# Optimization experiments

Hardware: AMD Instinct MI355X
Metric: run time of the kernel (lower is better)

The kernel has to match this reference:

```python
import jax, jax.numpy as jnp
import numpy as np

B, N = 2048, 4096

def setup_inputs() -> dict:
    key = jax.random.key(0)
    k1, k2, k3, k4, k5 = jax.random.split(key, 5)
    scale = 1.0 / np.sqrt(N)  # match nn.Linear init scale
    return {
        "t": jnp.zeros((1,), dtype=jnp.float32),
        "y": jax.random.uniform(k1, (B, N), dtype=jnp.float32),
        "W1": jax.random.normal(k2, (N, N), dtype=jnp.float32) * scale,
        "b1": jax.random.normal(k3, (N,), dtype=jnp.float32) * scale,
        "W2": jax.random.normal(k4, (N, N), dtype=jnp.float32) * scale,
        "b2": jax.random.normal(k5, (N,), dtype=jnp.float32) * scale,
    }

def reference(t, y, W1, b1, W2, b2):
    # out = fcc2(fcc1(y)) : two Linear layers (y @ W^T + b)
    h = y @ W1.T + b1            # [B, N]
    out = h @ W2.T + b2          # [B, N]
    # f = ones(N,1) @ y @ out^T  ==  dot(y, out) broadcast over N;
    # dydt = y * (out - dot(y, out))   (replicator equation)
    dot = jnp.sum(y * out, axis=-1, keepdims=True)  # [B, 1]
    return y * (out - dot)       # [B, N]
```

## Files before the change

### kernel.cpp

```cpp
#include <hip/hip_runtime.h>
#include <hip/hip_bf16.h>
#include <stdint.h>

typedef _Float16 f16;
typedef _Float16 f16x4 __attribute__((ext_vector_type(4)));
typedef _Float16 f16x8 __attribute__((ext_vector_type(8)));
typedef float f32x4 __attribute__((ext_vector_type(4)));

#define ASYNC_COPY16(gsrc, ldst)                                                   \
    __builtin_amdgcn_global_load_lds(                                              \
        (__attribute__((address_space(1))) void*)(gsrc),                           \
        (__attribute__((address_space(3))) void*)(ldst), 16, 0, 0)

__global__ __launch_bounds__(256) void cvt_f32_to_f16(const float* __restrict__ in,
                                                      f16* __restrict__ out, int n4) {
    int i = blockIdx.x * 256 + threadIdx.x;
    if (i >= n4) return;
    float4 v = ((const float4*)in)[i];
    f16x4 o;
    o.x = (f16)v.x; o.y = (f16)v.y; o.z = (f16)v.z; o.w = (f16)v.w;
    ((f16x4*)out)[i] = o;
}

__global__ __launch_bounds__(256) void cvt3_f32_to_f16(const float* __restrict__ y,
                                                       const float* __restrict__ W1,
                                                       const float* __restrict__ W2,
                                                       f16* __restrict__ yb,
                                                       f16* __restrict__ w1b,
                                                       f16* __restrict__ w2b,
                                                       int nY4, int nW4) {
    int i = blockIdx.x * 256 + threadIdx.x;
    const float* src;
    f16* dst;
    int off;
    if (i < nY4) {
        src = y; dst = yb; off = i;
    } else if (i < nY4 + nW4) {
        src = W1; dst = w1b; off = i - nY4;
    } else {
        src = W2; dst = w2b; off = i - nY4 - nW4;
        if (off >= nW4) return;
    }
    float4 v = ((const float4*)src)[off];
    f16x4 o;
    o.x = (f16)v.x; o.y = (f16)v.y; o.z = (f16)v.z; o.w = (f16)v.w;
    ((f16x4*)dst)[off] = o;
}

template <int STORE_F16>
__global__ __launch_bounds__(128) void gemm_bt(const f16* __restrict__ A,
                                               const f16* __restrict__ Bm,
                                               const float* __restrict__ bias,
                                               void* __restrict__ Cout,
                                               int M, int N, int K) {
    constexpr int BM = 128, BN = 64, BK = 32;
    __shared__ __align__(16) f16 sA[BM * BK];
    __shared__ __align__(16) f16 sB[BN * BK];

    const int tid  = threadIdx.x;
    const int lane = tid & 63;
    const int wave = tid >> 6;

    const int bm = blockIdx.y * BM;
    const int bn = blockIdx.x * BN;

    const int srow = tid >> 2;
    const int scol = (tid & 3) * 8;

    const f16* Aptr = A + (size_t)bm * K;
    const f16* Bptr = Bm + (size_t)bn * K;

    f32x4 acc[4][4] = {};

    const int quad = lane >> 4;
    const int l16  = lane & 15;

    for (int k0 = 0; k0 < K; k0 += BK) {
#pragma unroll
        for (int i = 0; i < 4; i++) {
            const int r = srow + 32 * i;
            ASYNC_COPY16(Aptr + (size_t)r * K + k0 + scol, &sA[r * BK + scol]);
        }
#pragma unroll
        for (int j = 0; j < 2; j++) {
            const int r = srow + 32 * j;
            ASYNC_COPY16(Bptr + (size_t)r * K + k0 + scol, &sB[r * BK + scol]);
        }
        __syncthreads();

        f16x8 af[4], bf[4];
#pragma unroll
        for (int mi = 0; mi < 4; mi++)
            af[mi] = *(const f16x8*)&sA[(wave * 64 + mi * 16 + l16) * BK + quad * 8];
#pragma unroll
        for (int ni = 0; ni < 4; ni++)
            bf[ni] = *(const f16x8*)&sB[(ni * 16 + l16) * BK + quad * 8];

#pragma unroll
        for (int mi = 0; mi < 4; mi++)
#pragma unroll
            for (int ni = 0; ni < 4; ni++)
                acc[mi][ni] = __builtin_amdgcn_mfma_f32_16x16x32_f16(af[mi], bf[ni],
                                                                     acc[mi][ni], 0, 0, 0);
        __syncthreads();
    }

#pragma unroll
    for (int ni = 0; ni < 4; ni++) {
        const int col = bn + ni * 16 + l16;
        const float bv = bias[col];
#pragma unroll
        for (int mi = 0; mi < 4; mi++) {
            const int row0 = bm + wave * 64 + mi * 16 + quad * 4;
#pragma unroll
            for (int r = 0; r < 4; r++) {
                float v = acc[mi][ni][r] + bv;
                if (STORE_F16)
                    ((f16*)Cout)[(size_t)(row0 + r) * N + col] = (f16)v;
                else
                    ((float*)Cout)[(size_t)(row0 + r) * N + col] = v;
            }
        }
    }
}

__global__ __launch_bounds__(256) void replicator(const float* __restrict__ y,
                                                  float* __restrict__ out, int N) {
    const int row = blockIdx.x;
    const float4* y4 = (const float4*)(y + (size_t)row * N);
    float4* o4 = (float4*)(out + (size_t)row * N);
    const int n4 = N / 4;

    float p = 0.f;
    for (int i = threadIdx.x; i < n4; i += 256) {
        float4 a = y4[i], b = o4[i];
        p += a.x * b.x + a.y * b.y + a.z * b.z + a.w * b.w;
    }
#pragma unroll
    for (int off = 32; off > 0; off >>= 1) p += __shfl_down(p, off, 64);

    __shared__ float sred[4];
    if ((threadIdx.x & 63) == 0) sred[threadIdx.x >> 6] = p;
    __syncthreads();
    const float dot = sred[0] + sred[1] + sred[2] + sred[3];

    for (int i = threadIdx.x; i < n4; i += 256) {
        float4 a = y4[i], b = o4[i];
        float4 r;
        r.x = a.x * (b.x - dot);
        r.y = a.y * (b.y - dot);
        r.z = a.z * (b.z - dot);
        r.w = a.w * (b.w - dot);
        o4[i] = r;
    }
}

extern "C" void kernel_launch(void* const* d_in, const int* in_sizes, int n_in,
                              void* d_out, int out_size, void* d_ws, size_t ws_size,
                              hipStream_t stream) {
    const float* y  = (const float*)d_in[1];
    const float* W1 = (const float*)d_in[2];
    const float* b1 = (const float*)d_in[3];
    const float* W2 = (const float*)d_in[4];
    const float* b2 = (const float*)d_in[5];

    const int N = in_sizes[3];
    const int B = in_sizes[1] / N;
    float* out = (float*)d_out;

    const size_t szY = (size_t)B * N;
    const size_t szW = (size_t)N * N;

    const int yn4 = (int)(szY / 4);
    const int wn4 = (int)(szW / 4);

    dim3 g1(N / 64, B / 128);

    const size_t need_big = (szY + 2 * szW + szY) * sizeof(f16);

    if (ws_size >= need_big) {
        f16* yb  = (f16*)d_ws;
        f16* w1b = yb + szY;
        f16* w2b = w1b + szW;
        f16* hb  = w2b + szW;

        const int tot4 = yn4 + 2 * wn4;
        cvt3_f32_to_f16<<<(tot4 + 255) / 256, 256, 0, stream>>>(y, W1, W2, yb, w1b, w2b,
                                                                yn4, wn4);
        gemm_bt<1><<<g1, 128, 0, stream>>>(yb, w1b, b1, hb, B, N, N);
        gemm_bt<0><<<g1, 128, 0, stream>>>(hb, w2b, b2, out, B, N, N);
    } else {
        f16* yb = (f16*)d_ws;
        f16* wb = yb + szY;
        f16* hb = wb + szW;

        cvt_f32_to_f16<<<yn4 / 256, 256, 0, stream>>>(y, yb, yn4);
        cvt_f32_to_f16<<<wn4 / 256, 256, 0, stream>>>(W1, wb, wn4);
        gemm_bt<1><<<g1, 128, 0, stream>>>(yb, wb, b1, hb, B, N, N);
        cvt_f32_to_f16<<<wn4 / 256, 256, 0, stream>>>(W2, wb, wn4);
        gemm_bt<0><<<g1, 128, 0, stream>>>(hb, wb, b2, out, B, N, N);
    }

    replicator<<<B, 256, 0, stream>>>(y, out, N);
}
```

Before: 433.3 us.

## Enlarge GEMM tiles, double-buffer LDS, and XOR-swizzle shared memory layout

The GEMM kernel moves from 128x64x32 tiles with 2 waves to 128x128x64 tiles with 4 waves in a 2x2 arrangement. LDS buffers are double-buffered so the async global-to-LDS copy of the next K-slice is issued before computing on the current one, removing one barrier per iteration. Shared memory segments are XOR-swizzled by row to avoid bank conflicts on the fragment reads. In exchange, LDS use and register pressure go up, and the grid has half as many blocks.

```diff
diff --git a/kernel.cpp b/kernel.cpp
--- a/kernel.cpp
+++ b/kernel.cpp
@@ -48,70 +48,106 @@
 }
 
 template <int STORE_F16>
-__global__ __launch_bounds__(128) void gemm_bt(const f16* __restrict__ A,
+__global__ __launch_bounds__(256) void gemm_bt(const f16* __restrict__ A,
                                                const f16* __restrict__ Bm,
                                                const float* __restrict__ bias,
                                                void* __restrict__ Cout,
                                                int M, int N, int K) {
-    constexpr int BM = 128, BN = 64, BK = 32;
-    __shared__ __align__(16) f16 sA[BM * BK];
-    __shared__ __align__(16) f16 sB[BN * BK];
-
-    const int tid  = threadIdx.x;
-    const int lane = tid & 63;
-    const int wave = tid >> 6;
+    constexpr int BM = 128, BN = 128, BK = 64;
+    __shared__ __align__(16) f16 sA[2][BM * BK];
+    __shared__ __align__(16) f16 sB[2][BN * BK];
+
+    const int tid   = threadIdx.x;
+    const int lane  = tid & 63;
+    const int wave  = tid >> 6;
+    const int waveM = wave >> 1;
+    const int waveN = wave & 1;
 
     const int bm = blockIdx.y * BM;
     const int bn = blockIdx.x * BN;
 
-    const int srow = tid >> 2;
-    const int scol = (tid & 3) * 8;
-
     const f16* Aptr = A + (size_t)bm * K;
     const f16* Bptr = Bm + (size_t)bn * K;
 
+    const int srow_lo = tid >> 3;
+    const int sseg    = tid & 7;
+
     f32x4 acc[4][4] = {};
 
     const int quad = lane >> 4;
     const int l16  = lane & 15;
 
-    for (int k0 = 0; k0 < K; k0 += BK) {
-#pragma unroll
-        for (int i = 0; i < 4; i++) {
-            const int r = srow + 32 * i;
-            ASYNC_COPY16(Aptr + (size_t)r * K + k0 + scol, &sA[r * BK + scol]);
-        }
-#pragma unroll
-        for (int j = 0; j < 2; j++) {
-            const int r = srow + 32 * j;
-            ASYNC_COPY16(Bptr + (size_t)r * K + k0 + scol, &sB[r * BK + scol]);
-        }
+    const int iters = K / BK;
+
+    {
+#pragma unroll
+        for (int j = 0; j < 4; j++) {
+            const int row = j * 32 + srow_lo;
+            const int seg = sseg ^ (row & 7);
+            ASYNC_COPY16(Aptr + (size_t)row * K + 0 + seg * 8, &sA[0][j * 2048 + tid * 8]);
+        }
+#pragma unroll
+        for (int j = 0; j < 4; j++) {
+            const int row = j * 32 + srow_lo;
+            const int seg = sseg ^ (row & 7);
+            ASYNC_COPY16(Bptr + (size_t)row * K + 0 + seg * 8, &sB[0][j * 2048 + tid * 8]);
+        }
+    }
+
+    int cur = 0;
+    for (int it = 0; it < iters; ++it) {
         __syncthreads();
 
-        f16x8 af[4], bf[4];
-#pragma unroll
-        for (int mi = 0; mi < 4; mi++)
-            af[mi] = *(const f16x8*)&sA[(wave * 64 + mi * 16 + l16) * BK + quad * 8];
-#pragma unroll
-        for (int ni = 0; ni < 4; ni++)
-            bf[ni] = *(const f16x8*)&sB[(ni * 16 + l16) * BK + quad * 8];
-
-#pragma unroll
-        for (int mi = 0; mi < 4; mi++)
-#pragma unroll
-            for (int ni = 0; ni < 4; ni++)
-                acc[mi][ni] = __builtin_amdgcn_mfma_f32_16x16x32_f16(af[mi], bf[ni],
-                                                                     acc[mi][ni], 0, 0, 0);
-        __syncthreads();
+        if (it + 1 < iters) {
+            const int k0 = (it + 1) * BK;
+#pragma unroll
+            for (int j = 0; j < 4; j++) {
+                const int row = j * 32 + srow_lo;
+                const int seg = sseg ^ (row & 7);
+                ASYNC_COPY16(Aptr + (size_t)row * K + k0 + seg * 8,
+                             &sA[cur ^ 1][j * 2048 + tid * 8]);
+            }
+#pragma unroll
+            for (int j = 0; j < 4; j++) {
+                const int row = j * 32 + srow_lo;
+                const int seg = sseg ^ (row & 7);
+                ASYNC_COPY16(Bptr + (size_t)row * K + k0 + seg * 8,
+                             &sB[cur ^ 1][j * 2048 + tid * 8]);
+            }
+        }
+
+#pragma unroll
+        for (int h = 0; h < 2; h++) {
+            f16x8 af[4], bf[4];
+#pragma unroll
+            for (int mi = 0; mi < 4; mi++) {
+                const int row = waveM * 64 + mi * 16 + l16;
+                const int seg = (h * 4 + quad) ^ (row & 7);
+                af[mi] = *(const f16x8*)&sA[cur][row * BK + seg * 8];
+            }
+#pragma unroll
+            for (int ni = 0; ni < 4; ni++) {
+                const int row = waveN * 64 + ni * 16 + l16;
+                const int seg = (h * 4 + quad) ^ (row & 7);
+                bf[ni] = *(const f16x8*)&sB[cur][row * BK + seg * 8];
+            }
+#pragma unroll
+            for (int mi = 0; mi < 4; mi++)
+#pragma unroll
+                for (int ni = 0; ni < 4; ni++)
+                    acc[mi][ni] = __builtin_amdgcn_mfma_f32_16x16x32_f16(af[mi], bf[ni],
+                                                                         acc[mi][ni], 0, 0, 0);
+        }
+        cur ^= 1;
     }
 
 #pragma unroll
     for (int ni = 0; ni < 4; ni++) {
-        const int col = bn + ni * 16 + l16;
+        const int col = bn + waveN * 64 + ni * 16 + l16;
         const float bv = bias[col];
 #pragma unroll
         for (int mi = 0; mi < 4; mi++) {
-            const int row0 = bm + wave * 64 + mi * 16 + quad * 4;
+            const int row0 = bm + waveM * 64 + mi * 16 + quad * 4;
 #pragma unroll
             for (int r = 0; r < 4; r++) {
                 float v = acc[mi][ni][r] + bv;
@@ -174,7 +210,7 @@
     const int yn4 = (int)(szY / 4);
     const int wn4 = (int)(szW / 4);
 
-    dim3 g1(N / 64, B / 128);
+    dim3 g1(N / 128, B / 128);
 
     const size_t need_big = (szY + 2 * szW + szY) * sizeof(f16);
 
@@ -187,8 +223,8 @@
         const int tot4 = yn4 + 2 * wn4;
         cvt3_f32_to_f16<<<(tot4 + 255) / 256, 256, 0, stream>>>(y, W1, W2, yb, w1b, w2b,
                                                                 yn4, wn4);
-        gemm_bt<1><<<g1, 128, 0, stream>>>(yb, w1b, b1, hb, B, N, N);
-        gemm_bt<0><<<g1, 128, 0, stream>>>(hb, w2b, b2, out, B, N, N);
+        gemm_bt<1><<<g1, 256, 0, stream>>>(yb, w1b, b1, hb, B, N, N);
+        gemm_bt<0><<<g1, 256, 0, stream>>>(hb, w2b, b2, out, B, N, N);
     } else {
         f16* yb = (f16*)d_ws;
         f16* wb = yb + szY;
@@ -196,9 +232,9 @@
 
         cvt_f32_to_f16<<<yn4 / 256, 256, 0, stream>>>(y, yb, yn4);
         cvt_f32_to_f16<<<wn4 / 256, 256, 0, stream>>>(W1, wb, wn4);
-        gemm_bt<1><<<g1, 128, 0, stream>>>(yb, wb, b1, hb, B, N, N);
+        gemm_bt<1><<<g1, 256, 0, stream>>>(yb, wb, b1, hb, B, N, N);
         cvt_f32_to_f16<<<wn4 / 256, 256, 0, stream>>>(W2, wb, wn4);
-        gemm_bt<0><<<g1, 128, 0, stream>>>(hb, wb, b2, out, B, N, N);
+        gemm_bt<0><<<g1, 256, 0, stream>>>(hb, wb, b2, out, B, N, N);
     }
 
     replicator<<<B, 256, 0, stream>>>(y, out, N);
```

After: 349.0 us. 19.5% less time.
